# Optimization experiments

Measured on AMD Instinct MI355X. Metric: run time of the kernel, lower is better.

## Reference

```python
import jax, jax.numpy as jnp
import numpy as np

IN_DIM = 64 * 64 + 8 * 24  # 4288 concatenated logits
OUT_DIM = 1858             # lc0 policy outputs


def _make_policy_map(seed=0):
    # Stand-in for apm.make_map(): fixed binary near-one-hot selection matrix.
    # Each of the 1858 policy outputs selects exactly one of the 4288 inputs.
    rng = np.random.default_rng(seed)
    sel = rng.integers(0, IN_DIM, size=OUT_DIM)
    m = np.zeros((IN_DIM, OUT_DIM), dtype=np.float32)
    m[sel, np.arange(OUT_DIM)] = 1.0
    return jnp.asarray(m)


def setup_inputs() -> dict:
    key = jax.random.key(0)
    k1, k2 = jax.random.split(key)
    B = 8192
    logits = jax.random.normal(k1, (B, 64, 64), dtype=jnp.float32)
    pp_logits = jax.random.normal(k2, (B, 8, 24), dtype=jnp.float32)
    fc1 = _make_policy_map()
    return {"logits": logits, "pp_logits": pp_logits, "fc1": fc1}


def reference(logits, pp_logits, fc1):
    B = logits.shape[0]
    flat = jnp.concatenate(
        [logits.reshape(B, 64 * 64), pp_logits.reshape(B, 8 * 24)], axis=1
    )  # [B, 4288]
    return jnp.matmul(flat, fc1.astype(flat.dtype))  # [B, 1858]
```

## Files before the change

### kernel.cpp

```cpp
#include <hip/hip_runtime.h>

#define IN_DIM     4288
#define LOGITS_DIM 4096
#define PP_DIM     192
#define OUT_DIM    1858
#define PADDED_OUT 2048
#define MAXNZ      8
#define OVF        (MAXNZ - 1)
#define OUT_G      (OUT_DIM / 4)
#define OUT_TAIL   (OUT_DIM - OUT_G * 4)

#define PAIR_OFF   1864
#define ZERO_WORDS (PAIR_OFF + 2 * PADDED_OUT)

__global__ void zero_ws_kernel(int* __restrict__ w) {
    int t = blockIdx.x * blockDim.x + threadIdx.x;
    if (t < ZERO_WORDS) w[t] = 0;
}

__global__ void build_csc_kernel(const float* __restrict__ fc1,
                                 int* __restrict__ cnt,
                                 int* __restrict__ flag,
                                 int2* __restrict__ pair,
                                 int* __restrict__ idxo,
                                 float* __restrict__ valo) {
    const long total4 = (long)IN_DIM * OUT_DIM / 4;
    const long stride = (long)gridDim.x * blockDim.x;
    for (long t = blockIdx.x * (long)blockDim.x + threadIdx.x; t < total4; t += stride) {
        float4 v = ((const float4*)fc1)[t];
        float vv[4] = {v.x, v.y, v.z, v.w};
        #pragma unroll
        for (int c = 0; c < 4; ++c) {
            if (vv[c] != 0.0f) {
                long e = t * 4 + c;
                int j = (int)(e % OUT_DIM);
                int i = (int)(e / OUT_DIM);
                int slot = atomicAdd(&cnt[j], 1);
                if (slot == 0) {
                    pair[j] = make_int2(i, __float_as_int(vv[c]));
                } else if (slot < MAXNZ) {
                    idxo[j * OVF + slot - 1] = i;
                    valo[j * OVF + slot - 1] = vv[c];
                    *flag = 1;
                }
            }
        }
    }
}

__global__ __launch_bounds__(256) void gather_kernel(
        const float* __restrict__ logits,
        const float* __restrict__ pp,
        const int*   __restrict__ flag,
        const int2*  __restrict__ pair,
        const int*   __restrict__ cnt,
        const int*   __restrict__ idxo,
        const float* __restrict__ valo,
        float*       __restrict__ out) {
    __shared__ float row[IN_DIM];
    const int b   = blockIdx.x;
    const int tid = threadIdx.x;

    const float4* lg4  = (const float4*)(logits + (size_t)b * LOGITS_DIM);
    float4*       row4 = (float4*)row;
    #pragma unroll
    for (int u = 0; u < 4; ++u) {
        __builtin_amdgcn_global_load_lds(
            (const __attribute__((address_space(1))) void*)(lg4 + tid + u * 256),
            (__attribute__((address_space(3))) void*)(row4 + tid + u * 256),
            16, 0, 0);
    }
    if (tid < PP_DIM / 4) {
        __builtin_amdgcn_global_load_lds(
            (const __attribute__((address_space(1))) void*)(((const float4*)(pp + (size_t)b * PP_DIM)) + tid),
            (__attribute__((address_space(3))) void*)(((float4*)(row + LOGITS_DIM)) + tid),
            16, 0, 0);
    }

    int4 rp01[2], rp23[2];
    #pragma unroll
    for (int u = 0; u < 2; ++u) {
        int g = tid + u * 256;
        rp01[u] = ((const int4*)pair)[2 * g];
        rp23[u] = ((const int4*)pair)[2 * g + 1];
    }
    const int of = *flag;

    __syncthreads();

    float* orow = out + (size_t)b * OUT_DIM;
    if (of == 0) {
        #pragma unroll
        for (int u = 0; u < 2; ++u) {
            int g = tid + u * 256;
            if (g < OUT_G) {
                float4 o;
                o.x = __int_as_float(rp01[u].y) * row[rp01[u].x];
                o.y = __int_as_float(rp01[u].w) * row[rp01[u].z];
                o.z = __int_as_float(rp23[u].y) * row[rp23[u].x];
                o.w = __int_as_float(rp23[u].w) * row[rp23[u].z];
                ((float4*)orow)[g] = o;
            } else if (g == OUT_G) {
                orow[4 * g]     = __int_as_float(rp01[u].y) * row[rp01[u].x];
                orow[4 * g + 1] = __int_as_float(rp01[u].w) * row[rp01[u].z];
            }
        }
    } else {
        #pragma unroll
        for (int u = 0; u < 2; ++u) {
            int g = tid + u * 256;
            int jv[4] = {rp01[u].x, rp01[u].z, rp23[u].x, rp23[u].z};
            int vv[4] = {rp01[u].y, rp01[u].w, rp23[u].y, rp23[u].w};
            #pragma unroll
            for (int e = 0; e < 4; ++e) {
                int j = 4 * g + e;
                if (j < OUT_DIM) {
                    float acc = __int_as_float(vv[e]) * row[jv[e]];
                    int c = cnt[j];
                    c = (c > MAXNZ ? MAXNZ : c) - 1;
                    for (int k = 0; k < c; ++k)
                        acc += valo[j * OVF + k] * row[idxo[j * OVF + k]];
                    orow[j] = acc;
                }
            }
        }
    }
}

extern "C" void kernel_launch(void* const* d_in, const int* in_sizes, int n_in,
                              void* d_out, int out_size, void* d_ws, size_t ws_size,
                              hipStream_t stream) {
    const float* logits = (const float*)d_in[0];
    const float* pp     = (const float*)d_in[1];
    const float* fc1    = (const float*)d_in[2];
    float* out = (float*)d_out;

    const int B = in_sizes[0] / LOGITS_DIM;

    int*   w    = (int*)d_ws;
    int*   cnt  = w;
    int*   flag = w + OUT_DIM;
    int2*  pair = (int2*)(w + PAIR_OFF);
    int*   idxo = (int*)(pair + PADDED_OUT);
    float* valo = (float*)(idxo + OUT_DIM * OVF);

    zero_ws_kernel<<<(ZERO_WORDS + 255) / 256, 256, 0, stream>>>(w);
    build_csc_kernel<<<1024, 256, 0, stream>>>(fc1, cnt, flag, pair, idxo, valo);
    gather_kernel<<<B, 256, 0, stream>>>(logits, pp, flag, pair, cnt, idxo, valo, out);
}
```

Before: 45.67 us.

## Process four batch rows per block with double-buffered LDS staging

The gather kernel now handles four consecutive batch rows per block. It keeps two shared-memory row buffers and issues the async global-to-LDS load for the next row before computing the current one. This is meant to overlap the row loads with the gather work and to amortize the per-block loads of the pair table and flag across rows. It doubles LDS use per block and cuts the grid to a quarter. The CSC build kernel's grid size is also doubled.

```diff
diff --git a/kernel.cpp b/kernel.cpp
--- a/kernel.cpp
+++ b/kernel.cpp
@@ -8,7 +8,7 @@
 #define MAXNZ      8
 #define OVF        (MAXNZ - 1)
 #define OUT_G      (OUT_DIM / 4)
-#define OUT_TAIL   (OUT_DIM - OUT_G * 4)
+#define ROWS       4
 
 #define PAIR_OFF   1864
 #define ZERO_WORDS (PAIR_OFF + 2 * PADDED_OUT)
@@ -48,19 +48,11 @@
     }
 }
 
-__global__ __launch_bounds__(256) void gather_kernel(
-        const float* __restrict__ logits,
-        const float* __restrict__ pp,
-        const int*   __restrict__ flag,
-        const int2*  __restrict__ pair,
-        const int*   __restrict__ cnt,
-        const int*   __restrict__ idxo,
-        const float* __restrict__ valo,
-        float*       __restrict__ out) {
-    __shared__ float row[IN_DIM];
-    const int b   = blockIdx.x;
-    const int tid = threadIdx.x;
 
+__device__ __forceinline__ void stage_row(const float* __restrict__ logits,
+                                          const float* __restrict__ pp,
+                                          float* __restrict__ row,
+                                          int b, int tid) {
     const float4* lg4  = (const float4*)(logits + (size_t)b * LOGITS_DIM);
     float4*       row4 = (float4*)row;
     #pragma unroll
@@ -76,19 +68,15 @@
             (__attribute__((address_space(3))) void*)(((float4*)(row + LOGITS_DIM)) + tid),
             16, 0, 0);
     }
+}
 
-    int4 rp01[2], rp23[2];
-    #pragma unroll
-    for (int u = 0; u < 2; ++u) {
-        int g = tid + u * 256;
-        rp01[u] = ((const int4*)pair)[2 * g];
-        rp23[u] = ((const int4*)pair)[2 * g + 1];
-    }
-    const int of = *flag;
-
-    __syncthreads();
-
-    float* orow = out + (size_t)b * OUT_DIM;
+__device__ __forceinline__ void compute_row(const float* __restrict__ row,
+                                            const int4* rp01, const int4* rp23,
+                                            int of, int tid,
+                                            const int* __restrict__ cnt,
+                                            const int* __restrict__ idxo,
+                                            const float* __restrict__ valo,
+                                            float* __restrict__ orow) {
     if (of == 0) {
         #pragma unroll
         for (int u = 0; u < 2; ++u) {
@@ -127,6 +115,47 @@
     }
 }
 
+__global__ __launch_bounds__(256) void gather_kernel(
+        const float* __restrict__ logits,
+        const float* __restrict__ pp,
+        const int*   __restrict__ flag,
+        const int2*  __restrict__ pair,
+        const int*   __restrict__ cnt,
+        const int*   __restrict__ idxo,
+        const float* __restrict__ valo,
+        float*       __restrict__ out,
+        int B) {
+    __shared__ float row[2][IN_DIM];
+    const int tid = threadIdx.x;
+    const int b0  = blockIdx.x * ROWS;
+
+    stage_row(logits, pp, row[0], b0, tid);
+
+    int4 rp01[2], rp23[2];
+    #pragma unroll
+    for (int u = 0; u < 2; ++u) {
+        int g = tid + u * 256;
+        rp01[u] = ((const int4*)pair)[2 * g];
+        rp23[u] = ((const int4*)pair)[2 * g + 1];
+    }
+    const int of = *flag;
+
+    __syncthreads();
+
+    int cur = 0;
+    #pragma unroll
+    for (int r = 0; r < ROWS; ++r) {
+        int b = b0 + r;
+        if (b >= B) break;
+        if (r + 1 < ROWS && b + 1 < B)
+            stage_row(logits, pp, row[cur ^ 1], b + 1, tid);
+        compute_row(row[cur], rp01, rp23, of, tid, cnt, idxo, valo,
+                    out + (size_t)b * OUT_DIM);
+        __syncthreads();
+        cur ^= 1;
+    }
+}
+
 extern "C" void kernel_launch(void* const* d_in, const int* in_sizes, int n_in,
                               void* d_out, int out_size, void* d_ws, size_t ws_size,
                               hipStream_t stream) {
@@ -135,7 +164,7 @@
     const float* fc1    = (const float*)d_in[2];
     float* out = (float*)d_out;
 
-    const int B = in_sizes[0] / LOGITS_DIM;
+    int B = in_sizes[0] / LOGITS_DIM;
 
     int*   w    = (int*)d_ws;
     int*   cnt  = w;
@@ -145,6 +174,7 @@
     float* valo = (float*)(idxo + OUT_DIM * OVF);
 
     zero_ws_kernel<<<(ZERO_WORDS + 255) / 256, 256, 0, stream>>>(w);
-    build_csc_kernel<<<1024, 256, 0, stream>>>(fc1, cnt, flag, pair, idxo, valo);
-    gather_kernel<<<B, 256, 0, stream>>>(logits, pp, flag, pair, cnt, idxo, valo, out);
+    build_csc_kernel<<<2048, 256, 0, stream>>>(fc1, cnt, flag, pair, idxo, valo);
+    gather_kernel<<<(B + ROWS - 1) / ROWS, 256, 0, stream>>>(
+        logits, pp, flag, pair, cnt, idxo, valo, out, B);
 }
```

Result: no change. 46.36 us (+1.5%).
